# Kernel optimization log

Measured on AMD Instinct MI355X. Metric: run time of the kernel, lower is better.

## Reference

```python
import jax, jax.numpy as jnp
import numpy as np

NUM_GROUPS = 32
EPS = 1e-6


def group_norm(x, weight, bias):
    # x: [b, c, h, w]
    b, c, h, w = x.shape
    xg = x.reshape(b, NUM_GROUPS, c // NUM_GROUPS, h, w)
    mean = jnp.mean(xg, axis=(2, 3, 4), keepdims=True)
    var = jnp.var(xg, axis=(2, 3, 4), keepdims=True)
    xn = ((xg - mean) * jax.lax.rsqrt(var + EPS)).reshape(b, c, h, w)
    return xn * weight[None, :, None, None] + bias[None, :, None, None]


def conv1x1(x, w, b):
    # 1x1 conv == per-pixel matmul. x: [b, c_in, h, w], w: [c_out, c_in]
    return jnp.einsum('oi,bihw->bohw', w, x) + b[None, :, None, None]


def setup_inputs() -> dict:
    key = jax.random.key(0)
    ks = jax.random.split(key, 9)
    b, c, h, w = 8, 512, 64, 64
    scale = 1.0 / np.sqrt(c)
    return {
        'x': jax.random.normal(ks[0], (b, c, h, w), jnp.float32),
        'gn_weight': jnp.ones((c,), jnp.float32),
        'gn_bias': jnp.zeros((c,), jnp.float32),
        'wq': jax.random.normal(ks[1], (c, c), jnp.float32) * scale,
        'bq': jnp.zeros((c,), jnp.float32),
        'wk': jax.random.normal(ks[2], (c, c), jnp.float32) * scale,
        'bk': jnp.zeros((c,), jnp.float32),
        'wv': jax.random.normal(ks[3], (c, c), jnp.float32) * scale,
        'bv': jnp.zeros((c,), jnp.float32),
        'wp': jax.random.normal(ks[4], (c, c), jnp.float32) * scale,
        'bp': jnp.zeros((c,), jnp.float32),
    }


def reference(x, gn_weight, gn_bias, wq, bq, wk, bk, wv, bv, wp, bp):
    h_ = group_norm(x, gn_weight, gn_bias)
    q = conv1x1(h_, wq, bq)
    k = conv1x1(h_, wk, bk)
    v = conv1x1(h_, wv, bv)
    b, c, h, w = q.shape
    n = h * w
    qf = q.reshape(b, c, n)
    kf = k.reshape(b, c, n)
    vf = v.reshape(b, c, n)
    # scores: [b, q, k]
    scores = jnp.einsum('bcq,bck->bqk', qf, kf) * (c ** -0.5)
    attn = jax.nn.softmax(scores, axis=-1)
    out = jnp.einsum('bqk,bck->bcq', attn, vf).reshape(b, c, h, w)
    out = conv1x1(out, wp, bp)
    return x + out
```

## Files before the change

### kernel.cpp

```cpp
#include <hip/hip_runtime.h>
#include <cstdint>

typedef unsigned short u16;
typedef __bf16 bf16x8 __attribute__((ext_vector_type(8)));
typedef float f32x4 __attribute__((ext_vector_type(4)));

__device__ __forceinline__ u16 f2bf(float f) {
    uint32_t u = __float_as_uint(f);
    u += 0x7FFFu + ((u >> 16) & 1u);
    return (u16)(u >> 16);
}
__device__ __forceinline__ float bf2f(u16 v) {
    return __uint_as_float((uint32_t)v << 16);
}

__device__ __forceinline__ void gload16(const u16* g, u16* l) {
    __builtin_amdgcn_global_load_lds(
        (const __attribute__((address_space(1))) uint32_t*)g,
        (__attribute__((address_space(3))) uint32_t*)l, 16, 0, 0);
}

__device__ __forceinline__ void swz(int& n_idx, int& m_idx, int& z_idx) {
    const int nx = gridDim.x, ny = gridDim.y;
    int lid = blockIdx.x + nx * (blockIdx.y + ny * blockIdx.z);
    int g = lid & 7, h = lid >> 3;
    n_idx = h % nx;
    int pair = (h / nx) * 8 + g;
    m_idx = pair % ny;
    z_idx = pair / ny;
}

__global__ __launch_bounds__(256) void k_detect(const u16* __restrict__ x,
                                                int* __restrict__ flag) {
    const int t = threadIdx.x;
    uint32_t mx = 0;
    for (int i = 0; i < 256; i++) {
        uint32_t v = (uint32_t)x[i * 256 + t] & 0x7FFFu;
        mx = mx > v ? mx : v;
    }
    for (int off = 32; off > 0; off >>= 1) {
        uint32_t o = (uint32_t)__shfl_xor((int)mx, off);
        mx = mx > o ? mx : o;
    }
    __shared__ uint32_t r[4];
    if ((t & 63) == 0) r[t >> 6] = mx;
    __syncthreads();
    if (t == 0) {
        uint32_t a = r[0] > r[1] ? r[0] : r[1];
        uint32_t b = r[2] > r[3] ? r[2] : r[3];
        mx = a > b ? a : b;
        *flag = (mx > 0x5000u) ? 1 : 0;
    }
}

__global__ __launch_bounds__(256) void k_cvt_wb(const void* wq, const void* wk,
                                                const void* wv, const void* wp,
                                                const void* gw, const void* gb,
                                                const void* bq, const void* bk,
                                                const void* bv, const void* bp,
                                                const int* __restrict__ flag,
                                                u16* __restrict__ Wc,
                                                u16* __restrict__ Bc) {
    const int mode = *flag;
    int i = blockIdx.x * 256 + threadIdx.x;
    if (i >= 1048576 + 3072) return;
    const void* src;
    u16* dst;
    int off;
    if (i < 1048576) {
        int which = i >> 18;
        off = i & 262143;
        src = which == 0 ? wq : which == 1 ? wk : which == 2 ? wv : wp;
        dst = Wc + i;
    } else {
        int j = i - 1048576;
        int which = j >> 9;
        off = j & 511;
        src = which == 0 ? gw : which == 1 ? gb : which == 2 ? bq
            : which == 3 ? bk : which == 4 ? bv : bp;
        dst = Bc + j;
    }
    *dst = mode ? f2bf(((const float*)src)[off]) : ((const u16*)src)[off];
}

__global__ __launch_bounds__(256) void k_gn_stats(const void* __restrict__ x_raw,
                                                  const u16* __restrict__ Bc,
                                                  const int* __restrict__ flag,
                                                  float* __restrict__ Sc,
                                                  float* __restrict__ Sh) {
    const int b = blockIdx.x >> 5, g = blockIdx.x & 31;
    const int mode = *flag;
    const int t = threadIdx.x;
    const int wave = t >> 6, lane = t & 63;
    float s = 0.f, ss = 0.f;
    if (mode) {
        const float4* xb = (const float4*)((const float*)x_raw +
                                           ((size_t)b * 512 + g * 16) * 4096);
        for (int it = 0; it < 64; it++) {
            float4 v = xb[it * 256 + t];
            s += v.x + v.y + v.z + v.w;
            ss += v.x * v.x + v.y * v.y + v.z * v.z + v.w * v.w;
        }
    } else {
        const uint4* xb = (const uint4*)((const u16*)x_raw +
                                         ((size_t)b * 512 + g * 16) * 4096);
        for (int it = 0; it < 32; it++) {
            uint4 v = xb[it * 256 + t];
            uint32_t w[4] = {v.x, v.y, v.z, v.w};
            for (int j = 0; j < 4; j++) {
                float a = __uint_as_float(w[j] << 16);
                float c = __uint_as_float(w[j] & 0xFFFF0000u);
                s += a + c;
                ss += a * a + c * c;
            }
        }
    }
    for (int off = 32; off > 0; off >>= 1) {
        s += __shfl_xor(s, off);
        ss += __shfl_xor(ss, off);
    }
    __shared__ float rs[4], rss[4];
    if (lane == 0) { rs[wave] = s; rss[wave] = ss; }
    __syncthreads();
    s = rs[0] + rs[1] + rs[2] + rs[3];
    ss = rss[0] + rss[1] + rss[2] + rss[3];
    const float mean = s * (1.f / 65536.f);
    const float var = ss * (1.f / 65536.f) - mean * mean;
    const float rstd = rsqrtf(var + 1e-6f);
    if (t < 16) {
        int c = g * 16 + t;
        float w = bf2f(Bc[c]);
        Sc[b * 512 + c] = rstd * w;
        Sh[b * 512 + c] = bf2f(Bc[512 + c]) - mean * rstd * w;
    }
}

#define TPAD 520
__global__ __launch_bounds__(256) void k_gn_apply(const void* __restrict__ x_raw,
                                                  const int* __restrict__ flag,
                                                  const float* __restrict__ Sc,
                                                  const float* __restrict__ Sh,
                                                  u16* __restrict__ HT) {
    __shared__ u16 tile[64 * TPAD];
    __shared__ float sSc[512], sSh[512];
    const int b = blockIdx.y;
    const int p0 = blockIdx.x * 64;
    const int mode = *flag;
    const int t = threadIdx.x;
    sSc[t] = Sc[b * 512 + t]; sSc[t + 256] = Sc[b * 512 + t + 256];
    sSh[t] = Sh[b * 512 + t]; sSh[t + 256] = Sh[b * 512 + t + 256];
    __syncthreads();
    for (int it = 0; it < 16; it++) {
        int li = it * 256 + t;
        int c = li >> 3;
        int pj = (li & 7) * 8;
        float v[8];
        if (mode) {
            const float* xr = (const float*)x_raw + ((size_t)b * 512 + c) * 4096 + p0 + pj;
            float4 a = *(const float4*)xr;
            float4 d = *(const float4*)(xr + 4);
            v[0] = a.x; v[1] = a.y; v[2] = a.z; v[3] = a.w;
            v[4] = d.x; v[5] = d.y; v[6] = d.z; v[7] = d.w;
        } else {
            const u16* xr = (const u16*)x_raw + ((size_t)b * 512 + c) * 4096 + p0 + pj;
            uint4 a = *(const uint4*)xr;
            uint32_t w[4] = {a.x, a.y, a.z, a.w};
            for (int j = 0; j < 4; j++) {
                v[2 * j] = __uint_as_float(w[j] << 16);
                v[2 * j + 1] = __uint_as_float(w[j] & 0xFFFF0000u);
            }
        }
        float sc = sSc[c], sh = sSh[c];
        for (int k = 0; k < 8; k++)
            tile[(pj + k) * TPAD + c] = f2bf(v[k] * sc + sh);
    }
    __syncthreads();
    u16* H = HT + (size_t)b * 2097152 + (size_t)p0 * 512;
    for (int it = 0; it < 16; it++) {
        int ch = it * 256 + t;
        int pp = ch >> 6;
        int cc = (ch & 63) * 8;
        *(uint4*)&H[(size_t)pp * 512 + cc] = *(const uint4*)&tile[pp * TPAD + cc];
    }
}

__device__ __forceinline__ void gemm_core(const u16* __restrict__ A,
                                          const u16* __restrict__ BT,
                                          int lda, int ldb, int K,
                                          int m0, int n0,
                                          u16* lA, u16* lB,
                                          f32x4 (&acc)[4][4]) {
    const int t = threadIdx.x;
    const int wave = t >> 6, lane = t & 63;
    const int wm = (wave >> 1) * 64, wn = (wave & 1) * 64;
    const int mf = lane & 15, quad = lane >> 4;
    const int srow = t >> 3;
    const int scol = (((t & 7) ^ (srow & 7)) * 8);
    const u16* Ap = A + (size_t)(m0 + srow) * lda + scol;
    const u16* Bp = BT + (size_t)(n0 + srow) * ldb + scol;
    u16* lAd = &lA[t * 8];
    u16* lBd = &lB[t * 8];
    const int fx = mf & 7;

    for (int i = 0; i < 4; i++)
        for (int j = 0; j < 4; j++)
            acc[i][j] = (f32x4){0.f, 0.f, 0.f, 0.f};

    for (int k0 = 0; k0 < K; k0 += 64) {
        __syncthreads();
        gload16(Ap + k0, lAd);
        gload16(Ap + k0 + (size_t)32 * lda, lAd + 2048);
        gload16(Ap + k0 + (size_t)64 * lda, lAd + 4096);
        gload16(Ap + k0 + (size_t)96 * lda, lAd + 6144);
        gload16(Bp + k0, lBd);
        gload16(Bp + k0 + (size_t)32 * ldb, lBd + 2048);
        gload16(Bp + k0 + (size_t)64 * ldb, lBd + 4096);
        gload16(Bp + k0 + (size_t)96 * ldb, lBd + 6144);
        __syncthreads();
        for (int ks = 0; ks < 2; ks++) {
            bf16x8 af[4], bfr[4];
            const int sl = ((ks * 4 + quad) ^ fx) * 8;
            for (int i = 0; i < 4; i++)
                af[i] = *(const bf16x8*)&lA[(wm + i * 16 + mf) * 64 + sl];
            for (int j = 0; j < 4; j++)
                bfr[j] = *(const bf16x8*)&lB[(wn + j * 16 + mf) * 64 + sl];
            for (int i = 0; i < 4; i++)
                for (int j = 0; j < 4; j++)
                    acc[i][j] = __builtin_amdgcn_mfma_f32_16x16x32_bf16(af[i], bfr[j], acc[i][j], 0, 0, 0);
        }
    }
}

__global__ __launch_bounds__(256) void k_qkv(const u16* __restrict__ HT,
                                             const u16* __restrict__ Wc,
                                             const u16* __restrict__ Bc,
                                             u16* __restrict__ QT,
                                             u16* __restrict__ KT,
                                             u16* __restrict__ V) {
    __shared__ __align__(16) u16 sm[16384];
    int nI, mI, zI;
    swz(nI, mI, zI);
    const int b = zI / 3, s = zI % 3;
    const u16* Bb = Bc + 1024 + s * 512;
    int m0, n0, ldo, bias_by_row;
    const u16 *A, *BT;
    u16* O;
    if (s < 2) {
        m0 = mI * 128; n0 = nI * 128;
        A = HT + (size_t)b * 2097152; BT = Wc + (size_t)s * 262144;
        O = (s == 0 ? QT : KT) + (size_t)b * 2097152; ldo = 512; bias_by_row = 0;
    } else {
        m0 = nI * 128; n0 = mI * 128;
        A = Wc + (size_t)2 * 262144; BT = HT + (size_t)b * 2097152;
        O = V + (size_t)b * 2097152; ldo = 4096; bias_by_row = 1;
    }
    f32x4 acc[4][4];
    gemm_core(A, BT, 512, 512, 512, m0, n0, sm, sm + 8192, acc);

    const int t = threadIdx.x;
    const int wave = t >> 6, lane = t & 63;
    const int wm = (wave >> 1) * 64, wn = (wave & 1) * 64;
    const int mf = lane & 15, quad = lane >> 4;
    __syncthreads();
    for (int i = 0; i < 4; i++)
        for (int r = 0; r < 4; r++) {
            int row = wm + i * 16 + quad * 4 + r;
            int kk = ((row >> 2) & 3) << 4;
            for (int j = 0; j < 4; j++) {
                int col = wn + j * 16 + mf;
                float bias = bf2f(Bb[bias_by_row ? (m0 + row) : (n0 + col)]);
                sm[row * 128 + (col ^ kk)] = f2bf(acc[i][j][r] + bias);
            }
        }
    __syncthreads();
    for (int p = 0; p < 8; p++) {
        int idx = p * 256 + t;
        int rowt = idx >> 4, c8 = (idx & 15) * 8;
        int kk = ((rowt >> 2) & 3) << 4;
        uint4 v = *(const uint4*)&sm[rowt * 128 + (c8 ^ kk)];
        *(uint4*)&O[(size_t)(m0 + rowt) * ldo + n0 + c8] = v;
    }
}

__device__ __forceinline__ u16* s_ptr(u16* S_ht, u16* S_tail, int l) {
    return l == 0 ? S_ht : S_tail + (size_t)(l - 1) * 16777216;
}

__global__ __launch_bounds__(256) void k_scores(const u16* __restrict__ QT,
                                                const u16* __restrict__ KT,
                                                u16* __restrict__ S_ht,
                                                u16* __restrict__ S_tail,
                                                float* __restrict__ Part,
                                                int b0) {
    __shared__ __align__(16) u16 sm[16384];
    int nI, mI, l;
    swz(nI, mI, l);
    const int n0 = nI * 128;
    const int m0 = mI * 128;
    const int b = b0 + l;
    f32x4 acc[4][4];
    gemm_core(QT + (size_t)b * 2097152, KT + (size_t)b * 2097152, 512, 512, 512,
              m0, n0, sm, sm + 8192, acc);

    const float scale = 0.04419417382415922f;
    const int t = threadIdx.x;
    const int wave = t >> 6, lane = t & 63;
    const int wm = (wave >> 1) * 64, wn = (wave & 1) * 64;
    const int mf = lane & 15, quad = lane >> 4;
    __syncthreads();
    for (int i = 0; i < 4; i++)
        for (int r = 0; r < 4; r++) {
            int row = wm + i * 16 + quad * 4 + r;
            int kk = ((row >> 2) & 3) << 4;
            for (int j = 0; j < 4; j++) {
                int col = wn + j * 16 + mf;
                sm[row * 128 + (col ^ kk)] = f2bf(__expf(acc[i][j][r] * scale));
            }
        }
    __syncthreads();
    u16* Sb = s_ptr(S_ht, S_tail, l);
    float* pr = Part + ((size_t)b * 32 + nI) * 4096 + m0;
    for (int p = 0; p < 8; p++) {
        int idx = p * 256 + t;
        int rowt = idx >> 4, c8 = (idx & 15) * 8;
        int kk = ((rowt >> 2) & 3) << 4;
        uint4 v = *(const uint4*)&sm[rowt * 128 + (c8 ^ kk)];
        uint32_t w[4] = {v.x, v.y, v.z, v.w};
        float s = 0.f;
        for (int q2 = 0; q2 < 4; q2++)
            s += __uint_as_float(w[q2] << 16) + __uint_as_float(w[q2] & 0xFFFF0000u);
        for (int off = 8; off > 0; off >>= 1) s += __shfl_xor(s, off);
        if ((lane & 15) == 0) pr[rowt] = s;
        *(uint4*)&Sb[(size_t)(m0 + rowt) * 4096 + n0 + c8] = v;
    }
}

__global__ __launch_bounds__(256) void k_pv_split(u16* __restrict__ S_ht,
                                                  u16* __restrict__ S_tail,
                                                  const u16* __restrict__ V,
                                                  u16* __restrict__ QT,
                                                  u16* __restrict__ KT,
                                                  int b0) {
    __shared__ __align__(16) u16 sm[16384];
    int nI, mI, zI;
    swz(nI, mI, zI);
    const int n0 = nI * 128;
    const int m0 = mI * 128;
    const int l = zI >> 1, split = zI & 1, b = b0 + l;
    const u16* A = s_ptr(S_ht, S_tail, l) + split * 2048;
    const u16* BT = V + (size_t)b * 2097152 + split * 2048;
    f32x4 acc[4][4];
    gemm_core(A, BT, 4096, 4096, 2048, m0, n0, sm, sm + 8192, acc);

    const int t = threadIdx.x;
    const int wave = t >> 6, lane = t & 63;
    const int wm = (wave >> 1) * 64, wn = (wave & 1) * 64;
    const int mf = lane & 15, quad = lane >> 4;
    u16* P = (split == 0 ? QT : KT) + (size_t)b * 2097152;
    __syncthreads();
    for (int i = 0; i < 4; i++)
        for (int r = 0; r < 4; r++) {
            int row = wm + i * 16 + quad * 4 + r;
            int kk = ((row >> 2) & 3) << 4;
            for (int j = 0; j < 4; j++) {
                int col = wn + j * 16 + mf;
                sm[row * 128 + (col ^ kk)] = f2bf(acc[i][j][r]);
            }
        }
    __syncthreads();
    for (int p = 0; p < 8; p++) {
        int idx = p * 256 + t;
        int rowt = idx >> 4, c8 = (idx & 15) * 8;
        int kk = ((rowt >> 2) & 3) << 4;
        uint4 v = *(const uint4*)&sm[rowt * 128 + (c8 ^ kk)];
        *(uint4*)&P[(size_t)(m0 + rowt) * 512 + n0 + c8] = v;
    }
}

__global__ __launch_bounds__(256) void k_pv_reduce(const u16* __restrict__ QT,
                                                   const u16* __restrict__ KT,
                                                   const float* __restrict__ Part,
                                                   u16* __restrict__ OT,
                                                   int b0) {
    const int b = b0 + blockIdx.y;
    const int t = threadIdx.x;
    __shared__ float sInv[4];
    if (t < 128) {
        int r = t >> 5, which = t & 31;
        int p = blockIdx.x * 4 + r;
        float v = Part[((size_t)b * 32 + which) * 4096 + p];
        for (int off = 16; off > 0; off >>= 1) v += __shfl_xor(v, off);
        if (which == 0) sInv[r] = 1.f / v;
    }
    __syncthreads();
    const float inv = sInv[t >> 6];
    size_t base = (size_t)b * 2097152;
    size_t i0 = base + ((size_t)blockIdx.x * 256 + t) * 8;
    uint4 a = *(const uint4*)(QT + i0);
    uint4 c = *(const uint4*)(KT + i0);
    uint32_t wa[4] = {a.x, a.y, a.z, a.w};
    uint32_t wc[4] = {c.x, c.y, c.z, c.w};
    uint32_t o[4];
    for (int j = 0; j < 4; j++) {
        float lo = (__uint_as_float(wa[j] << 16) + __uint_as_float(wc[j] << 16)) * inv;
        float hi = (__uint_as_float(wa[j] & 0xFFFF0000u) + __uint_as_float(wc[j] & 0xFFFF0000u)) * inv;
        o[j] = (uint32_t)f2bf(lo) | ((uint32_t)f2bf(hi) << 16);
    }
    *(uint4*)(OT + i0) = make_uint4(o[0], o[1], o[2], o[3]);
}

__global__ __launch_bounds__(256) void k_proj(const u16* __restrict__ Wc,
                                              const u16* __restrict__ OT,
                                              const u16* __restrict__ Bc,
                                              const void* __restrict__ x_raw,
                                              const int* __restrict__ flag,
                                              void* __restrict__ y_raw) {
    __shared__ __align__(16) u16 smu[16384];
    float* smf = (float*)smu;
    int nI, mI, b;
    swz(nI, mI, b);
    const int n0 = nI * 128;
    const int m0 = mI * 128;
    f32x4 acc[4][4];
    gemm_core(Wc + (size_t)3 * 262144, OT + (size_t)b * 2097152, 512, 512, 512,
              m0, n0, smu, smu + 8192, acc);

    const int mode = *flag;
    const u16* bp = Bc + 5 * 512;
    const int t = threadIdx.x;
    const int wave = t >> 6, lane = t & 63;
    const int wn = (wave & 1) * 64;
    const int mf = lane & 15, quad = lane >> 4;
    const int whalf = wave >> 1;
    size_t bb = (size_t)b * 2097152;
    for (int h = 0; h < 2; h++) {
        __syncthreads();
        if (whalf == h) {
            for (int i = 0; i < 4; i++)
                for (int r = 0; r < 4; r++) {
                    int rowl = i * 16 + quad * 4 + r;
                    int kf = ((rowl >> 2) & 1) << 4;
                    for (int j = 0; j < 4; j++) {
                        int col = wn + j * 16 + mf;
                        smf[rowl * 128 + (col ^ kf)] = acc[i][j][r];
                    }
                }
        }
        __syncthreads();
        const int rowbase = m0 + h * 64;
        if (mode) {
            for (int p = 0; p < 8; p++) {
                int idx = p * 256 + t;
                int rowl = idx >> 5, c4 = (idx & 31) * 4;
                int kf = ((rowl >> 2) & 1) << 4;
                f32x4 v = *(const f32x4*)&smf[rowl * 128 + (c4 ^ kf)];
                int rowg = rowbase + rowl;
                float bias = bf2f(bp[rowg]);
                size_t o = bb + (size_t)rowg * 4096 + n0 + c4;
                float4 xv = *(const float4*)((const float*)x_raw + o);
                float4 out = make_float4(v[0] + bias + xv.x, v[1] + bias + xv.y,
                                         v[2] + bias + xv.z, v[3] + bias + xv.w);
                *(float4*)((float*)y_raw + o) = out;
            }
        } else {
            for (int p = 0; p < 4; p++) {
                int idx = p * 256 + t;
                int rowl = idx >> 4, c8 = (idx & 15) * 8;
                int kf = ((rowl >> 2) & 1) << 4;
                const float* sp = &smf[rowl * 128 + (c8 ^ kf)];
                f32x4 v0 = *(const f32x4*)sp;
                f32x4 v1 = *(const f32x4*)(sp + 4);
                int rowg = rowbase + rowl;
                float bias = bf2f(bp[rowg]);
                size_t o = bb + (size_t)rowg * 4096 + n0 + c8;
                uint4 xv = *(const uint4*)((const u16*)x_raw + o);
                uint32_t xw[4] = {xv.x, xv.y, xv.z, xv.w};
                float vals[8] = {v0[0], v0[1], v0[2], v0[3],
                                 v1[0], v1[1], v1[2], v1[3]};
                uint32_t ow[4];
                for (int q2 = 0; q2 < 4; q2++) {
                    float lo = __uint_as_float(xw[q2] << 16) + vals[2 * q2] + bias;
                    float hi = __uint_as_float(xw[q2] & 0xFFFF0000u) + vals[2 * q2 + 1] + bias;
                    ow[q2] = (uint32_t)f2bf(lo) | ((uint32_t)f2bf(hi) << 16);
                }
                *(uint4*)((u16*)y_raw + o) = make_uint4(ow[0], ow[1], ow[2], ow[3]);
            }
        }
    }
}

extern "C" void kernel_launch(void* const* d_in, const int* in_sizes, int n_in,
                              void* d_out, int out_size, void* d_ws, size_t ws_size,
                              hipStream_t stream) {
    (void)in_sizes; (void)n_in; (void)out_size;
    const void* x  = d_in[0];
    const void* gw = d_in[1];
    const void* gb = d_in[2];
    const void* wq = d_in[3];
    const void* bq = d_in[4];
    const void* wk = d_in[5];
    const void* bk = d_in[6];
    const void* wv = d_in[7];
    const void* bv = d_in[8];
    const void* wp = d_in[9];
    const void* bp = d_in[10];

    u16* ws16 = (u16*)d_ws;
    int* flag = (int*)d_ws;
    float* Sc = (float*)(ws16 + 16);
    float* Sh = Sc + 4096;
    u16* Wc = ws16 + 16 + 16384;
    u16* Bc = Wc + 1048576;
    u16* HT = Bc + 4096;
    u16* QT = HT + 16777216;
    u16* KT = QT + 16777216;
    u16* V  = KT + 16777216;
    u16* OT = V  + 16777216;
    float* Part = (float*)(OT + 16777216);
    u16* Tail = (u16*)(Part + 1048576);
    const size_t base_elems = (size_t)(Tail - ws16);

    int nb = 1;
    for (int cand = 8; cand >= 2; cand >>= 1) {
        size_t need = 2ull * (base_elems + (size_t)(cand - 1) * 16777216ull);
        if (ws_size >= need) { nb = cand; break; }
    }

    k_detect<<<1, 256, 0, stream>>>((const u16*)x, flag);
    k_cvt_wb<<<4108, 256, 0, stream>>>(wq, wk, wv, wp, gw, gb, bq, bk, bv, bp,
                                       flag, Wc, Bc);
    k_gn_stats<<<256, 256, 0, stream>>>(x, Bc, flag, Sc, Sh);
    k_gn_apply<<<dim3(64, 8), 256, 0, stream>>>(x, flag, Sc, Sh, HT);
    k_qkv<<<dim3(4, 32, 24), 256, 0, stream>>>(HT, Wc, Bc, QT, KT, V);
    for (int b0 = 0; b0 < 8; b0 += nb) {
        k_scores<<<dim3(32, 32, nb), 256, 0, stream>>>(QT, KT, HT, Tail, Part, b0);
        k_pv_split<<<dim3(4, 32, 2 * nb), 256, 0, stream>>>(HT, Tail, V, QT, KT, b0);
        k_pv_reduce<<<dim3(1024, nb), 256, 0, stream>>>(QT, KT, Part, OT, b0);
    }
    k_proj<<<dim3(32, 4, 8), 256, 0, stream>>>(Wc, OT, Bc, x, flag, d_out);
}
```

Before: 759.1 us.

## Enlarge scores GEMM tile to 256x256 with 512 threads and interleaved prefetch

Rewrites the QK^T scores kernel to use 256x256 output tiles computed by 8 waves, with a hand-scheduled double-buffered LDS pipeline that interleaves async global-to-LDS prefetch with MFMA blocks and uses setprio. The row-sum partials now come from 16 column tiles instead of 32, so the reduce kernel is adjusted to match. The goal is more data reuse per loaded tile and overlap of loads with MFMA work. In exchange it uses 128KB of LDS and many accumulator registers, which limits occupancy.

Result: faster. 722.4 us (-4.8%).

```diff
diff --git a/kernel.cpp b/kernel.cpp
--- a/kernel.cpp
+++ b/kernel.cpp
@@ -286,52 +286,158 @@
     return l == 0 ? S_ht : S_tail + (size_t)(l - 1) * 16777216;
 }
 
-__global__ __launch_bounds__(256) void k_scores(const u16* __restrict__ QT,
-                                                const u16* __restrict__ KT,
-                                                u16* __restrict__ S_ht,
-                                                u16* __restrict__ S_tail,
-                                                float* __restrict__ Part,
-                                                int b0) {
-    __shared__ __align__(16) u16 sm[16384];
+__global__ __launch_bounds__(512, 2) void k_scores(const u16* __restrict__ QT,
+                                                   const u16* __restrict__ KT,
+                                                   u16* __restrict__ S_ht,
+                                                   u16* __restrict__ S_tail,
+                                                   float* __restrict__ Part,
+                                                   int b0) {
+    __shared__ __align__(16) u16 lds[65536];
     int nI, mI, l;
     swz(nI, mI, l);
-    const int n0 = nI * 128;
-    const int m0 = mI * 128;
+    const int n0 = nI * 256;
+    const int m0 = mI * 256;
     const int b = b0 + l;
-    f32x4 acc[4][4];
-    gemm_core(QT + (size_t)b * 2097152, KT + (size_t)b * 2097152, 512, 512, 512,
-              m0, n0, sm, sm + 8192, acc);
+    const u16* Aq = QT + (size_t)b * 2097152;
+    const u16* Bk = KT + (size_t)b * 2097152;
+
+    const int t = threadIdx.x;
+    const int wave = t >> 6, lane = t & 63;
+    const int wm = (wave >> 2) * 128, wn = (wave & 3) * 64;
+    const int mf = lane & 15, quad = lane >> 4;
+    const int fx = mf & 7;
+    const int srow = t >> 3;
+    const int scol8 = t & 7;
+
+    f32x4 acc[8][4];
+#pragma unroll
+    for (int i = 0; i < 8; i++)
+#pragma unroll
+        for (int j = 0; j < 4; j++)
+            acc[i][j] = (f32x4){0.f, 0.f, 0.f, 0.f};
+
+    auto issueA = [&](u16* dst, int h, int k0) {
+#pragma unroll
+        for (int s = 0; s < 2; s++) {
+            int row = h * 128 + s * 64 + srow;
+            gload16(Aq + (size_t)(m0 + row) * 512 + k0 + ((scol8 ^ (row & 7)) << 3),
+                    dst + h * 8192 + s * 4096 + t * 8);
+        }
+    };
+    auto issueB = [&](u16* dst, int h, int k0) {
+#pragma unroll
+        for (int s = 0; s < 2; s++) {
+            int row = h * 128 + s * 64 + srow;
+            gload16(Bk + (size_t)(n0 + row) * 512 + k0 + ((scol8 ^ (row & 7)) << 3),
+                    dst + h * 8192 + s * 4096 + t * 8);
+        }
+    };
+
+    issueA(lds, 0, 0); issueA(lds, 1, 0);
+    issueB(lds + 16384, 0, 0); issueB(lds + 16384, 1, 0);
+
+    for (int kt = 0; kt < 8; kt++) {
+        u16* lA = (kt & 1) ? lds + 32768 : lds;
+        u16* lB = lA + 16384;
+        u16* pA = (kt & 1) ? lds : lds + 32768;
+        u16* pB = pA + 16384;
+        const int k0n = (kt + 1) << 6;
+        const bool pf = kt < 7;
+        asm volatile("" ::: "memory");
+        __builtin_amdgcn_s_barrier();
+        asm volatile("" ::: "memory");
+        if (pf) {
+            issueA(pA, 0, k0n);
+            asm volatile("s_waitcnt vmcnt(2)" ::: "memory");
+        } else {
+            asm volatile("s_waitcnt vmcnt(0)" ::: "memory");
+        }
+        __builtin_amdgcn_s_barrier();
+        asm volatile("" ::: "memory");
+
+        bf16x8 af[8], bfr[2];
+        int sl = (quad ^ fx) * 8;
+#pragma unroll
+        for (int i = 0; i < 8; i++)
+            af[i] = *(const bf16x8*)&lA[(wm + i * 16 + mf) * 64 + sl];
+#pragma unroll
+        for (int j = 0; j < 2; j++)
+            bfr[j] = *(const bf16x8*)&lB[(wn + j * 16 + mf) * 64 + sl];
+        __builtin_amdgcn_s_setprio(1);
+#pragma unroll
+        for (int i = 0; i < 8; i++)
+#pragma unroll
+            for (int j = 0; j < 2; j++)
+                acc[i][j] = __builtin_amdgcn_mfma_f32_16x16x32_bf16(af[i], bfr[j], acc[i][j], 0, 0, 0);
+        __builtin_amdgcn_s_setprio(0);
+        if (pf) issueA(pA, 1, k0n);
+#pragma unroll
+        for (int j = 0; j < 2; j++)
+            bfr[j] = *(const bf16x8*)&lB[(wn + (2 + j) * 16 + mf) * 64 + sl];
+        __builtin_amdgcn_s_setprio(1);
+#pragma unroll
+        for (int i = 0; i < 8; i++)
+#pragma unroll
+            for (int j = 0; j < 2; j++)
+                acc[i][2 + j] = __builtin_amdgcn_mfma_f32_16x16x32_bf16(af[i], bfr[j], acc[i][2 + j], 0, 0, 0);
+        __builtin_amdgcn_s_setprio(0);
+        sl = ((4 + quad) ^ fx) * 8;
+        if (pf) issueB(pB, 0, k0n);
+#pragma unroll
+        for (int i = 0; i < 8; i++)
+            af[i] = *(const bf16x8*)&lA[(wm + i * 16 + mf) * 64 + sl];
+#pragma unroll
+        for (int j = 0; j < 2; j++)
+            bfr[j] = *(const bf16x8*)&lB[(wn + j * 16 + mf) * 64 + sl];
+        __builtin_amdgcn_s_setprio(1);
+#pragma unroll
+        for (int i = 0; i < 8; i++)
+#pragma unroll
+            for (int j = 0; j < 2; j++)
+                acc[i][j] = __builtin_amdgcn_mfma_f32_16x16x32_bf16(af[i], bfr[j], acc[i][j], 0, 0, 0);
+        __builtin_amdgcn_s_setprio(0);
+        if (pf) issueB(pB, 1, k0n);
+#pragma unroll
+        for (int j = 0; j < 2; j++)
+            bfr[j] = *(const bf16x8*)&lB[(wn + (2 + j) * 16 + mf) * 64 + sl];
+        __builtin_amdgcn_s_setprio(1);
+#pragma unroll
+        for (int i = 0; i < 8; i++)
+#pragma unroll
+            for (int j = 0; j < 2; j++)
+                acc[i][2 + j] = __builtin_amdgcn_mfma_f32_16x16x32_bf16(af[i], bfr[j], acc[i][2 + j], 0, 0, 0);
+        __builtin_amdgcn_s_setprio(0);
+    }
 
     const float scale = 0.04419417382415922f;
-    const int t = threadIdx.x;
-    const int wave = t >> 6, lane = t & 63;
-    const int wm = (wave >> 1) * 64, wn = (wave & 1) * 64;
-    const int mf = lane & 15, quad = lane >> 4;
-    __syncthreads();
-    for (int i = 0; i < 4; i++)
+    __syncthreads();
+#pragma unroll
+    for (int i = 0; i < 8; i++)
+#pragma unroll
         for (int r = 0; r < 4; r++) {
             int row = wm + i * 16 + quad * 4 + r;
-            int kk = ((row >> 2) & 3) << 4;
+            int key = row & 7;
+#pragma unroll
             for (int j = 0; j < 4; j++) {
                 int col = wn + j * 16 + mf;
-                sm[row * 128 + (col ^ kk)] = f2bf(__expf(acc[i][j][r] * scale));
+                lds[row * 256 + (((col >> 3) ^ key) << 3) + (col & 7)] =
+                    f2bf(__expf(acc[i][j][r] * scale));
             }
         }
     __syncthreads();
     u16* Sb = s_ptr(S_ht, S_tail, l);
-    float* pr = Part + ((size_t)b * 32 + nI) * 4096 + m0;
-    for (int p = 0; p < 8; p++) {
-        int idx = p * 256 + t;
-        int rowt = idx >> 4, c8 = (idx & 15) * 8;
-        int kk = ((rowt >> 2) & 3) << 4;
-        uint4 v = *(const uint4*)&sm[rowt * 128 + (c8 ^ kk)];
+    float* pr = Part + ((size_t)b * 16 + nI) * 4096 + m0;
+    for (int p = 0; p < 16; p++) {
+        int idx = p * 512 + t;
+        int row = idx >> 5, chunk = idx & 31;
+        uint4 v = *(const uint4*)&lds[row * 256 + ((chunk ^ (row & 7)) << 3)];
         uint32_t w[4] = {v.x, v.y, v.z, v.w};
         float s = 0.f;
         for (int q2 = 0; q2 < 4; q2++)
             s += __uint_as_float(w[q2] << 16) + __uint_as_float(w[q2] & 0xFFFF0000u);
-        for (int off = 8; off > 0; off >>= 1) s += __shfl_xor(s, off);
-        if ((lane & 15) == 0) pr[rowt] = s;
-        *(uint4*)&Sb[(size_t)(m0 + rowt) * 4096 + n0 + c8] = v;
+        for (int off = 16; off > 0; off >>= 1) s += __shfl_xor(s, off);
+        if ((lane & 31) == 0) pr[row] = s;
+        *(uint4*)&Sb[(size_t)(m0 + row) * 4096 + n0 + chunk * 8] = v;
     }
 }
 
@@ -385,11 +491,11 @@
     const int b = b0 + blockIdx.y;
     const int t = threadIdx.x;
     __shared__ float sInv[4];
-    if (t < 128) {
-        int r = t >> 5, which = t & 31;
+    if (t < 64) {
+        int r = t >> 4, which = t & 15;
         int p = blockIdx.x * 4 + r;
-        float v = Part[((size_t)b * 32 + which) * 4096 + p];
-        for (int off = 16; off > 0; off >>= 1) v += __shfl_xor(v, off);
+        float v = Part[((size_t)b * 16 + which) * 4096 + p];
+        for (int off = 8; off > 0; off >>= 1) v += __shfl_xor(v, off);
         if (which == 0) sInv[r] = 1.f / v;
     }
     __syncthreads();
@@ -533,7 +639,7 @@
     k_gn_apply<<<dim3(64, 8), 256, 0, stream>>>(x, flag, Sc, Sh, HT);
     k_qkv<<<dim3(4, 32, 24), 256, 0, stream>>>(HT, Wc, Bc, QT, KT, V);
     for (int b0 = 0; b0 < 8; b0 += nb) {
-        k_scores<<<dim3(32, 32, nb), 256, 0, stream>>>(QT, KT, HT, Tail, Part, b0);
+        k_scores<<<dim3(16, 16, nb), 512, 0, stream>>>(QT, KT, HT, Tail, Part, b0);
         k_pv_split<<<dim3(4, 32, 2 * nb), 256, 0, stream>>>(HT, Tail, V, QT, KT, b0);
         k_pv_reduce<<<dim3(1024, nb), 256, 0, stream>>>(QT, KT, Part, OT, b0);
     }
```
